# Optimization experiments

Hardware: AMD Instinct MI355X
Metric: run time of the kernel (lower is better)

The kernel has to match this reference:

```python
import jax, jax.numpy as jnp
import numpy as np

HEAD_SIZE = 64


def setup_inputs() -> dict:
    key = jax.random.key(0)
    ks = jax.random.split(key, 4)
    B, S, H, D = 8, 4096, 768, HEAD_SIZE
    scale = 1.0 / np.sqrt(H)
    return {
        "x": jax.random.normal(ks[0], (B, S, H), dtype=jnp.float32),
        "Wq": jax.random.normal(ks[1], (H, D), dtype=jnp.float32) * scale,
        "bq": jnp.zeros((D,), dtype=jnp.float32),
        "Wk": jax.random.normal(ks[2], (H, D), dtype=jnp.float32) * scale,
        "bk": jnp.zeros((D,), dtype=jnp.float32),
        "Wv": jax.random.normal(ks[3], (H, D), dtype=jnp.float32) * scale,
        "bv": jnp.zeros((D,), dtype=jnp.float32),
    }


def reference(x, Wq, bq, Wk, bk, Wv, bv):
    # x: [B, S, H]
    B, S, H = x.shape
    D = Wq.shape[1]
    q = x @ Wq + bq  # [B, S, D]
    k = x @ Wk + bk
    v = x @ Wv + bv
    # naive full score matrix [B, S, S]
    scores = jnp.einsum("bsd,btd->bst", q, k)
    causal = jnp.tril(jnp.ones((S, S), dtype=bool))  # lower-triangular mask
    scores = jnp.where(causal[None, :, :], scores, -jnp.inf)
    attn = jax.nn.softmax(scores / jnp.sqrt(jnp.float32(D)), axis=-1)
    # dropout is identity in eval/deterministic reference
    out = jnp.einsum("bst,btd->bsd", attn, v)  # [B, S, D]
    return out
```

## Files before the change

kernel.cpp:

```cpp
#include <hip/hip_runtime.h>

typedef unsigned short u16;
typedef __bf16 bf16_t;
typedef bf16_t bf16x8 __attribute__((ext_vector_type(8)));
typedef float f32x4 __attribute__((ext_vector_type(4)));
typedef u16 u16x8 __attribute__((ext_vector_type(8)));
typedef u16 u16x4 __attribute__((ext_vector_type(4)));

#define B_ 8
#define S_ 4096
#define H_ 768
#define M_ (B_ * S_)

__device__ __forceinline__ u16 f2b(float f) {
  unsigned u = __float_as_uint(f);
  u += 0x7fffu + ((u >> 16) & 1u);
  return (u16)(u >> 16);
}

__device__ __forceinline__ void gl_lds16(const void* g, void* l) {
  __builtin_amdgcn_global_load_lds(
      (const __attribute__((address_space(1))) void*)g,
      (__attribute__((address_space(3))) void*)l, 16, 0, 0);
}

__global__ __launch_bounds__(256) void wconv_k(const float* __restrict__ Wq,
                                               const float* __restrict__ Wk,
                                               const float* __restrict__ Wv,
                                               u16* __restrict__ WbT) {
  __shared__ float wt[64 * 68];
  const int tid = threadIdx.x;
  int mat = blockIdx.x / 12;
  int k0 = (blockIdx.x % 12) * 64;
  const float* W = (mat == 0) ? Wq : ((mat == 1) ? Wk : Wv);
  int r = tid >> 2, c0 = (tid & 3) * 16;
  const float* src = W + (size_t)(k0 + r) * 64 + c0;
#pragma unroll
  for (int j = 0; j < 16; j += 4)
    *(float4*)&wt[r * 68 + c0 + j] = *(const float4*)(src + j);
  __syncthreads();
  int d = tid >> 2;
  u16* dst = WbT + (size_t)(mat * 64 + d) * 768 + k0 + c0;
  u16x8 o0, o1;
#pragma unroll
  for (int j = 0; j < 8; ++j) o0[j] = f2b(wt[(c0 + j) * 68 + d]);
#pragma unroll
  for (int j = 0; j < 8; ++j) o1[j] = f2b(wt[(c0 + 8 + j) * 68 + d]);
  *(u16x8*)dst = o0;
  *(u16x8*)(dst + 8) = o1;
}

__global__ __launch_bounds__(256) void qkv_k(const float* __restrict__ x,
                                             const u16* __restrict__ WbT,
                                             const float* __restrict__ bq,
                                             const float* __restrict__ bk,
                                             const float* __restrict__ bv,
                                             u16* __restrict__ qb,
                                             u16* __restrict__ kb,
                                             u16* __restrict__ vbT) {
  __shared__ __align__(16) u16 smem[2 * 2560 + 2 * 7680];
  const int tid = threadIdx.x;
  const int w = tid >> 6, ln = tid & 15, qd = (tid >> 4) & 3;
  const int row0 = blockIdx.x * 64;

  const f32x4 z4 = {0.f, 0.f, 0.f, 0.f};
  f32x4 acc[4][3];
#pragma unroll
  for (int rt = 0; rt < 4; ++rt)
#pragma unroll
    for (int ct = 0; ct < 3; ++ct) acc[rt][ct] = z4;

  const int xr = tid >> 2, xc = (tid & 3) * 8;
  float4 xf0, xf1;
  u16x8 wf[3];

  auto load_t = [&](int kt) {
    const float* sx = x + (size_t)(row0 + xr) * 768 + kt * 32 + xc;
    xf0 = *(const float4*)sx;
    xf1 = *(const float4*)(sx + 4);
#pragma unroll
    for (int i = 0; i < 3; ++i) {
      int c = i * 256 + tid;
      int r = c >> 2, off = (c & 3) * 8;
      wf[i] = *(const u16x8*)(WbT + (size_t)r * 768 + kt * 32 + off);
    }
  };
  auto write_b = [&](int kt) {
    u16* xs = smem + (kt & 1) * 2560;
    u16* wsb = smem + 5120 + (kt & 1) * 7680;
    u16x8 v;
    v[0] = f2b(xf0.x); v[1] = f2b(xf0.y); v[2] = f2b(xf0.z); v[3] = f2b(xf0.w);
    v[4] = f2b(xf1.x); v[5] = f2b(xf1.y); v[6] = f2b(xf1.z); v[7] = f2b(xf1.w);
    *(u16x8*)&xs[xr * 40 + xc] = v;
#pragma unroll
    for (int i = 0; i < 3; ++i) {
      int c = i * 256 + tid;
      int r = c >> 2, off = (c & 3) * 8;
      *(u16x8*)&wsb[r * 40 + off] = wf[i];
    }
  };

  load_t(0);
  write_b(0);
  load_t(1);
  for (int kt = 0; kt < 24; ++kt) {
    __syncthreads();
    if (kt < 23) {
      write_b(kt + 1);
      if (kt < 22) load_t(kt + 2);
    }
    u16* xs = smem + (kt & 1) * 2560;
    u16* wsb = smem + 5120 + (kt & 1) * 7680;
    bf16x8 af[4], bfr[3];
#pragma unroll
    for (int rt = 0; rt < 4; ++rt)
      af[rt] = *(const bf16x8*)&xs[(rt * 16 + ln) * 40 + qd * 8];
#pragma unroll
    for (int ct = 0; ct < 3; ++ct)
      bfr[ct] = *(const bf16x8*)&wsb[(w * 48 + ct * 16 + ln) * 40 + qd * 8];
#pragma unroll
    for (int rt = 0; rt < 4; ++rt)
#pragma unroll
      for (int ct = 0; ct < 3; ++ct)
        acc[rt][ct] = __builtin_amdgcn_mfma_f32_16x16x32_bf16(
            af[rt], bfr[ct], acc[rt][ct], 0, 0, 0);
    __syncthreads();
  }

  u16* vt = smem;
#pragma unroll
  for (int ct = 0; ct < 3; ++ct) {
    int col = w * 48 + ct * 16 + ln;
    int mat = col >> 6, d = col & 63;
    if (mat < 2) {
      const float* bp = (mat == 0) ? bq : bk;
      u16* op = (mat == 0) ? qb : kb;
      float bias = bp[d];
      float scale = (mat == 0) ? 0.18033688011112042f : 1.0f;
#pragma unroll
      for (int rt = 0; rt < 4; ++rt)
#pragma unroll
        for (int r = 0; r < 4; ++r)
          op[(size_t)(row0 + rt * 16 + qd * 4 + r) * 64 + d] =
              f2b((acc[rt][ct][r] + bias) * scale);
    } else {
      float bias = bv[d];
#pragma unroll
      for (int rt = 0; rt < 4; ++rt)
#pragma unroll
        for (int r = 0; r < 4; ++r)
          vt[d * 72 + rt * 16 + qd * 4 + r] = f2b(acc[rt][ct][r] + bias);
    }
  }
  __syncthreads();
  {
    int d = tid >> 2, so = (tid & 3) * 16;
    int b = row0 >> 12, s0 = row0 & 4095;
    u16* dst = vbT + ((size_t)b * 64 + d) * 4096 + s0 + so;
    *(u16x8*)dst = *(const u16x8*)&vt[d * 72 + so];
    *(u16x8*)(dst + 8) = *(const u16x8*)&vt[d * 72 + so + 8];
  }
}

__global__ __launch_bounds__(256, 2) void attn_k(const u16* __restrict__ qb,
                                                 const u16* __restrict__ kb,
                                                 const u16* __restrict__ vbT,
                                                 u16* __restrict__ po,
                                                 float* __restrict__ pl) {
  __shared__ __align__(16) u16 ks[2][4096];
  __shared__ __align__(16) u16 vs[2][4096];
  __shared__ __align__(16) u16 ps[4 * 16 * 72];
  const int tid = threadIdx.x;
  const int w = tid >> 6, ln = tid & 15, qd = (tid >> 4) & 3;
  const int id = blockIdx.x;
  const int b = id & 7;
  int t = id >> 3;
  int qi = 15, rem = t;
  for (;;) {
    int c = (4 * qi + 11) >> 3;
    if (rem < c) break;
    rem -= c;
    --qi;
  }
  const int chunk = rem;
  const int tstart = rem * 8;
  int tcount = 4 * qi + 4 - tstart;
  if (tcount > 8) tcount = 8;
  const int q0 = qi * 256, q0w = q0 + w * 64;
  const int base = b * S_;
  const u16* kg = kb + (size_t)base * 64;
  const u16* vg = vbT + (size_t)b * 64 * 4096;

  bf16x8 qf[4][2];
#pragma unroll
  for (int qt = 0; qt < 4; ++qt) {
    const u16* qrow = qb + (size_t)(base + q0w + qt * 16 + ln) * 64;
    qf[qt][0] = *(const bf16x8*)(qrow + qd * 8);
    qf[qt][1] = *(const bf16x8*)(qrow + 32 + qd * 8);
  }
  const f32x4 z4 = {0.f, 0.f, 0.f, 0.f};
  f32x4 o[4][4];
#pragma unroll
  for (int qt = 0; qt < 4; ++qt)
#pragma unroll
    for (int nt = 0; nt < 4; ++nt) o[qt][nt] = z4;
  float lp[4] = {0.f, 0.f, 0.f, 0.f};
  u16* psw = ps + w * (16 * 72);
  const int lr = (tid & 63) >> 3, csl = tid & 7;

  auto prefetch = [&](int bufi, int tile) {
    const u16* kt_ = kg + (size_t)tile * 4096;
    const u16* vt_ = vg + tile * 64;
#pragma unroll
    for (int i = 0; i < 2; ++i) {
      int r0 = w * 16 + i * 8;
      int r = r0 + lr;
      int c = csl ^ (r & 7);
      gl_lds16(kt_ + r * 64 + c * 8, &ks[bufi][r0 * 64]);
      gl_lds16(vt_ + (size_t)r * 4096 + c * 8, &vs[bufi][r0 * 64]);
    }
  };

  prefetch(0, tstart);
  int buf = 0;
  for (int it = 0; it < tcount; ++it) {
    __syncthreads();
    if (it + 1 < tcount) prefetch(buf ^ 1, tstart + it + 1);
    const int t0a = (tstart + it) * 64;

    bf16x8 kf[2][4], vf[2][4];
#pragma unroll
    for (int kc = 0; kc < 2; ++kc) {
      int cs = ((kc * 4 + qd) ^ (ln & 7)) * 8;
#pragma unroll
      for (int nt = 0; nt < 4; ++nt) {
        kf[kc][nt] = *(const bf16x8*)&ks[buf][(nt * 16 + ln) * 64 + cs];
        vf[kc][nt] = *(const bf16x8*)&vs[buf][(nt * 16 + ln) * 64 + cs];
      }
    }
#pragma unroll
    for (int qt = 0; qt < 4; ++qt) {
      f32x4 s[4] = {z4, z4, z4, z4};
#pragma unroll
      for (int kc = 0; kc < 2; ++kc)
#pragma unroll
        for (int nt = 0; nt < 4; ++nt)
          s[nt] = __builtin_amdgcn_mfma_f32_16x16x32_bf16(kf[kc][nt], qf[qt][kc],
                                                          s[nt], 0, 0, 0);
      if (t0a + 63 > q0w + qt * 16) {
#pragma unroll
        for (int nt = 0; nt < 4; ++nt) {
          int tg = t0a + nt * 16 + qd * 4;
          int qg = q0w + qt * 16 + ln;
#pragma unroll
          for (int r = 0; r < 4; ++r)
            if (tg + r > qg) s[nt][r] = -INFINITY;
        }
      }
#pragma unroll
      for (int nt = 0; nt < 4; ++nt) {
        u16x4 pk;
#pragma unroll
        for (int r = 0; r < 4; ++r) {
          float p = __builtin_amdgcn_exp2f(s[nt][r]);
          lp[qt] += p;
          pk[r] = f2b(p);
        }
        *(u16x4*)&psw[ln * 72 + nt * 16 + qd * 4] = pk;
      }
#pragma unroll
      for (int kc = 0; kc < 2; ++kc) {
        bf16x8 pf = *(const bf16x8*)&psw[ln * 72 + kc * 32 + qd * 8];
#pragma unroll
        for (int nt = 0; nt < 4; ++nt)
          o[qt][nt] = __builtin_amdgcn_mfma_f32_16x16x32_bf16(vf[kc][nt], pf,
                                                              o[qt][nt], 0, 0, 0);
      }
    }
    buf ^= 1;
  }

  u16* poc = po + (size_t)chunk * M_ * 64;
  float* plc = pl + (size_t)chunk * M_;
#pragma unroll
  for (int qt = 0; qt < 4; ++qt) {
    float v = lp[qt];
    v += __shfl_xor(v, 16);
    v += __shfl_xor(v, 32);
    int row = base + q0w + qt * 16 + ln;
#pragma unroll
    for (int nt = 0; nt < 4; ++nt) {
      u16x4 ov;
#pragma unroll
      for (int r = 0; r < 4; ++r) ov[r] = f2b(o[qt][nt][r]);
      *(u16x4*)&poc[(size_t)row * 64 + nt * 16 + qd * 4] = ov;
    }
    if (qd == 0) plc[row] = v;
  }
}

__global__ __launch_bounds__(256) void comb_k(const u16* __restrict__ po,
                                              const float* __restrict__ pl,
                                              float* __restrict__ out) {
  int idx = blockIdx.x * 256 + threadIdx.x;
  int r = idx >> 4, d0 = (idx & 15) * 4;
  int qi = (r & 4095) >> 8;
  int nch = (4 * qi + 11) >> 3;
  float4 a = {0.f, 0.f, 0.f, 0.f};
  float l = 0.f;
  for (int c = 0; c < nch; ++c) {
    u16x4 p = *(const u16x4*)(po + ((size_t)c * M_ + r) * 64 + d0);
    a.x += __uint_as_float((unsigned)p[0] << 16);
    a.y += __uint_as_float((unsigned)p[1] << 16);
    a.z += __uint_as_float((unsigned)p[2] << 16);
    a.w += __uint_as_float((unsigned)p[3] << 16);
    l += pl[(size_t)c * M_ + r];
  }
  float inv = 1.0f / l;
  a.x *= inv; a.y *= inv; a.z *= inv; a.w *= inv;
  *(float4*)(out + (size_t)r * 64 + d0) = a;
}

extern "C" void kernel_launch(void* const* d_in, const int* in_sizes, int n_in,
                              void* d_out, int out_size, void* d_ws, size_t ws_size,
                              hipStream_t stream) {
  const float* x  = (const float*)d_in[0];
  const float* Wq = (const float*)d_in[1];
  const float* bq = (const float*)d_in[2];
  const float* Wk = (const float*)d_in[3];
  const float* bk = (const float*)d_in[4];
  const float* Wv = (const float*)d_in[5];
  const float* bv = (const float*)d_in[6];
  float* out = (float*)d_out;

  char* wsp = (char*)d_ws;
  u16* WbT  = (u16*)wsp;
  u16* qb   = (u16*)(wsp + 294912);
  u16* kb   = (u16*)(wsp + 4489216);
  u16* vbT  = (u16*)(wsp + 8683520);
  u16* po   = (u16*)(wsp + 12877824);
  float* pl = (float*)(wsp + 46432256);

  hipLaunchKernelGGL(wconv_k, dim3(36), dim3(256), 0, stream, Wq, Wk, Wv, WbT);
  hipLaunchKernelGGL(qkv_k, dim3(512), dim3(256), 0, stream,
                     x, WbT, bq, bk, bv, qb, kb, vbT);
  hipLaunchKernelGGL(attn_k, dim3(576), dim3(256), 0, stream,
                     qb, kb, vbT, po, pl);
  hipLaunchKernelGGL(comb_k, dim3(2048), dim3(256), 0, stream, po, pl, out);
}
```

Baseline: 230.8 us.

## Drop LDS staging in QKV and attention, load MFMA fragments directly from global

The QKV projection kernel drops its double-buffered LDS tiles. Each wave now loads x rows and all 192 weight columns straight into registers and accumulates a 16x192 strip, with a higher occupancy hint. V is stored in a per-64-token tiled transposed layout so the attention kernel can fetch K and V fragments directly from global memory into register double buffers (A/B ping-pong) instead of global_load_lds into swizzled LDS. This removes barriers and LDS traffic but relies on L1/L2 to serve the redundant per-wave global loads, and it raises register pressure.

```diff
diff --git a/kernel.cpp b/kernel.cpp
--- a/kernel.cpp
+++ b/kernel.cpp
@@ -16,12 +16,6 @@
   unsigned u = __float_as_uint(f);
   u += 0x7fffu + ((u >> 16) & 1u);
   return (u16)(u >> 16);
-}
-
-__device__ __forceinline__ void gl_lds16(const void* g, void* l) {
-  __builtin_amdgcn_global_load_lds(
-      (const __attribute__((address_space(1))) void*)g,
-      (__attribute__((address_space(3))) void*)l, 16, 0, 0);
 }
 
 __global__ __launch_bounds__(256) void wconv_k(const float* __restrict__ Wq,
@@ -50,125 +44,84 @@
   *(u16x8*)(dst + 8) = o1;
 }
 
-__global__ __launch_bounds__(256) void qkv_k(const float* __restrict__ x,
-                                             const u16* __restrict__ WbT,
-                                             const float* __restrict__ bq,
-                                             const float* __restrict__ bk,
-                                             const float* __restrict__ bv,
-                                             u16* __restrict__ qb,
-                                             u16* __restrict__ kb,
-                                             u16* __restrict__ vbT) {
-  __shared__ __align__(16) u16 smem[2 * 2560 + 2 * 7680];
+__global__ __launch_bounds__(256, 4) void qkv_k(const float* __restrict__ x,
+                                                const u16* __restrict__ WbT,
+                                                const float* __restrict__ bq,
+                                                const float* __restrict__ bk,
+                                                const float* __restrict__ bv,
+                                                u16* __restrict__ qb,
+                                                u16* __restrict__ kb,
+                                                u16* __restrict__ vbT2) {
+  __shared__ __align__(16) u16 vt[64 * 72];
   const int tid = threadIdx.x;
   const int w = tid >> 6, ln = tid & 15, qd = (tid >> 4) & 3;
-  const int row0 = blockIdx.x * 64;
+  const int r0 = blockIdx.x * 64 + w * 16;
 
   const f32x4 z4 = {0.f, 0.f, 0.f, 0.f};
-  f32x4 acc[4][3];
-#pragma unroll
-  for (int rt = 0; rt < 4; ++rt)
-#pragma unroll
-    for (int ct = 0; ct < 3; ++ct) acc[rt][ct] = z4;
-
-  const int xr = tid >> 2, xc = (tid & 3) * 8;
-  float4 xf0, xf1;
-  u16x8 wf[3];
-
-  auto load_t = [&](int kt) {
-    const float* sx = x + (size_t)(row0 + xr) * 768 + kt * 32 + xc;
-    xf0 = *(const float4*)sx;
-    xf1 = *(const float4*)(sx + 4);
-#pragma unroll
-    for (int i = 0; i < 3; ++i) {
-      int c = i * 256 + tid;
-      int r = c >> 2, off = (c & 3) * 8;
-      wf[i] = *(const u16x8*)(WbT + (size_t)r * 768 + kt * 32 + off);
-    }
-  };
-  auto write_b = [&](int kt) {
-    u16* xs = smem + (kt & 1) * 2560;
-    u16* wsb = smem + 5120 + (kt & 1) * 7680;
-    u16x8 v;
-    v[0] = f2b(xf0.x); v[1] = f2b(xf0.y); v[2] = f2b(xf0.z); v[3] = f2b(xf0.w);
-    v[4] = f2b(xf1.x); v[5] = f2b(xf1.y); v[6] = f2b(xf1.z); v[7] = f2b(xf1.w);
-    *(u16x8*)&xs[xr * 40 + xc] = v;
-#pragma unroll
-    for (int i = 0; i < 3; ++i) {
-      int c = i * 256 + tid;
-      int r = c >> 2, off = (c & 3) * 8;
-      *(u16x8*)&wsb[r * 40 + off] = wf[i];
-    }
-  };
-
-  load_t(0);
-  write_b(0);
-  load_t(1);
+  f32x4 acc[12];
+#pragma unroll
+  for (int ct = 0; ct < 12; ++ct) acc[ct] = z4;
+
+  const float* xrow = x + (size_t)(r0 + ln) * 768 + qd * 8;
+  const u16* wrow = WbT + (size_t)ln * 768 + qd * 8;
+
   for (int kt = 0; kt < 24; ++kt) {
-    __syncthreads();
-    if (kt < 23) {
-      write_b(kt + 1);
-      if (kt < 22) load_t(kt + 2);
-    }
-    u16* xs = smem + (kt & 1) * 2560;
-    u16* wsb = smem + 5120 + (kt & 1) * 7680;
-    bf16x8 af[4], bfr[3];
-#pragma unroll
-    for (int rt = 0; rt < 4; ++rt)
-      af[rt] = *(const bf16x8*)&xs[(rt * 16 + ln) * 40 + qd * 8];
-#pragma unroll
-    for (int ct = 0; ct < 3; ++ct)
-      bfr[ct] = *(const bf16x8*)&wsb[(w * 48 + ct * 16 + ln) * 40 + qd * 8];
-#pragma unroll
-    for (int rt = 0; rt < 4; ++rt)
-#pragma unroll
-      for (int ct = 0; ct < 3; ++ct)
-        acc[rt][ct] = __builtin_amdgcn_mfma_f32_16x16x32_bf16(
-            af[rt], bfr[ct], acc[rt][ct], 0, 0, 0);
-    __syncthreads();
-  }
-
-  u16* vt = smem;
-#pragma unroll
-  for (int ct = 0; ct < 3; ++ct) {
-    int col = w * 48 + ct * 16 + ln;
-    int mat = col >> 6, d = col & 63;
-    if (mat < 2) {
-      const float* bp = (mat == 0) ? bq : bk;
-      u16* op = (mat == 0) ? qb : kb;
-      float bias = bp[d];
-      float scale = (mat == 0) ? 0.18033688011112042f : 1.0f;
-#pragma unroll
-      for (int rt = 0; rt < 4; ++rt)
-#pragma unroll
-        for (int r = 0; r < 4; ++r)
-          op[(size_t)(row0 + rt * 16 + qd * 4 + r) * 64 + d] =
-              f2b((acc[rt][ct][r] + bias) * scale);
-    } else {
-      float bias = bv[d];
-#pragma unroll
-      for (int rt = 0; rt < 4; ++rt)
-#pragma unroll
-        for (int r = 0; r < 4; ++r)
-          vt[d * 72 + rt * 16 + qd * 4 + r] = f2b(acc[rt][ct][r] + bias);
-    }
+    float4 a0 = *(const float4*)(xrow + kt * 32);
+    float4 a1 = *(const float4*)(xrow + kt * 32 + 4);
+    u16x8 wv[12];
+#pragma unroll
+    for (int ct = 0; ct < 12; ++ct)
+      wv[ct] = *(const u16x8*)(wrow + (size_t)ct * 12288 + kt * 32);
+    u16x8 af;
+    af[0] = f2b(a0.x); af[1] = f2b(a0.y); af[2] = f2b(a0.z); af[3] = f2b(a0.w);
+    af[4] = f2b(a1.x); af[5] = f2b(a1.y); af[6] = f2b(a1.z); af[7] = f2b(a1.w);
+    bf16x8 afb = (bf16x8)af;
+#pragma unroll
+    for (int ct = 0; ct < 12; ++ct)
+      acc[ct] = __builtin_amdgcn_mfma_f32_16x16x32_bf16(afb, (bf16x8)wv[ct],
+                                                        acc[ct], 0, 0, 0);
+  }
+
+  const float scq = 0.18033688011112042f;
+#pragma unroll
+  for (int ct = 0; ct < 4; ++ct) {
+    float bias = bq[ct * 16 + ln];
+#pragma unroll
+    for (int r = 0; r < 4; ++r)
+      qb[(size_t)(r0 + qd * 4 + r) * 64 + ct * 16 + ln] =
+          f2b((acc[ct][r] + bias) * scq);
+  }
+#pragma unroll
+  for (int ct = 4; ct < 8; ++ct) {
+    float bias = bk[(ct - 4) * 16 + ln];
+#pragma unroll
+    for (int r = 0; r < 4; ++r)
+      kb[(size_t)(r0 + qd * 4 + r) * 64 + (ct - 4) * 16 + ln] =
+          f2b(acc[ct][r] + bias);
+  }
+#pragma unroll
+  for (int ct = 8; ct < 12; ++ct) {
+    float bias = bv[(ct - 8) * 16 + ln];
+    int d = (ct - 8) * 16 + ln;
+#pragma unroll
+    for (int r = 0; r < 4; ++r)
+      vt[d * 72 + w * 16 + qd * 4 + r] = f2b(acc[ct][r] + bias);
   }
   __syncthreads();
   {
-    int d = tid >> 2, so = (tid & 3) * 16;
-    int b = row0 >> 12, s0 = row0 & 4095;
-    u16* dst = vbT + ((size_t)b * 64 + d) * 4096 + s0 + so;
-    *(u16x8*)dst = *(const u16x8*)&vt[d * 72 + so];
-    *(u16x8*)(dst + 8) = *(const u16x8*)&vt[d * 72 + so + 8];
+    int d = tid >> 2, t0l = (tid & 3) * 16;
+    int b = blockIdx.x >> 6, ti = blockIdx.x & 63;
+    u16* dst = vbT2 + (size_t)(b * 64 + ti) * 4096 + d * 64 + t0l;
+    *(u16x8*)dst = *(const u16x8*)&vt[d * 72 + t0l];
+    *(u16x8*)(dst + 8) = *(const u16x8*)&vt[d * 72 + t0l + 8];
   }
 }
 
 __global__ __launch_bounds__(256, 2) void attn_k(const u16* __restrict__ qb,
                                                  const u16* __restrict__ kb,
-                                                 const u16* __restrict__ vbT,
+                                                 const u16* __restrict__ vbT2,
                                                  u16* __restrict__ po,
                                                  float* __restrict__ pl) {
-  __shared__ __align__(16) u16 ks[2][4096];
-  __shared__ __align__(16) u16 vs[2][4096];
   __shared__ __align__(16) u16 ps[4 * 16 * 72];
   const int tid = threadIdx.x;
   const int w = tid >> 6, ln = tid & 15, qd = (tid >> 4) & 3;
@@ -189,7 +142,7 @@
   const int q0 = qi * 256, q0w = q0 + w * 64;
   const int base = b * S_;
   const u16* kg = kb + (size_t)base * 64;
-  const u16* vg = vbT + (size_t)b * 64 * 4096;
+  const u16* vg = vbT2 + (size_t)b * 64 * 4096;
 
   bf16x8 qf[4][2];
 #pragma unroll
@@ -206,38 +159,22 @@
     for (int nt = 0; nt < 4; ++nt) o[qt][nt] = z4;
   float lp[4] = {0.f, 0.f, 0.f, 0.f};
   u16* psw = ps + w * (16 * 72);
-  const int lr = (tid & 63) >> 3, csl = tid & 7;
-
-  auto prefetch = [&](int bufi, int tile) {
+
+  bf16x8 kA[2][4], vA[2][4], kB[2][4], vB[2][4];
+
+  auto ldtile = [&](bf16x8(&kf)[2][4], bf16x8(&vf)[2][4], int tile) {
     const u16* kt_ = kg + (size_t)tile * 4096;
-    const u16* vt_ = vg + tile * 64;
-#pragma unroll
-    for (int i = 0; i < 2; ++i) {
-      int r0 = w * 16 + i * 8;
-      int r = r0 + lr;
-      int c = csl ^ (r & 7);
-      gl_lds16(kt_ + r * 64 + c * 8, &ks[bufi][r0 * 64]);
-      gl_lds16(vt_ + (size_t)r * 4096 + c * 8, &vs[bufi][r0 * 64]);
-    }
+    const u16* vt_ = vg + (size_t)tile * 4096;
+#pragma unroll
+    for (int kc = 0; kc < 2; ++kc)
+#pragma unroll
+      for (int nt = 0; nt < 4; ++nt) {
+        kf[kc][nt] = *(const bf16x8*)(kt_ + (nt * 16 + ln) * 64 + kc * 32 + qd * 8);
+        vf[kc][nt] = *(const bf16x8*)(vt_ + (nt * 16 + ln) * 64 + kc * 32 + qd * 8);
+      }
   };
 
-  prefetch(0, tstart);
-  int buf = 0;
-  for (int it = 0; it < tcount; ++it) {
-    __syncthreads();
-    if (it + 1 < tcount) prefetch(buf ^ 1, tstart + it + 1);
-    const int t0a = (tstart + it) * 64;
-
-    bf16x8 kf[2][4], vf[2][4];
-#pragma unroll
-    for (int kc = 0; kc < 2; ++kc) {
-      int cs = ((kc * 4 + qd) ^ (ln & 7)) * 8;
-#pragma unroll
-      for (int nt = 0; nt < 4; ++nt) {
-        kf[kc][nt] = *(const bf16x8*)&ks[buf][(nt * 16 + ln) * 64 + cs];
-        vf[kc][nt] = *(const bf16x8*)&vs[buf][(nt * 16 + ln) * 64 + cs];
-      }
-    }
+  auto body = [&](const bf16x8(&kf)[2][4], const bf16x8(&vf)[2][4], int t0a) {
 #pragma unroll
     for (int qt = 0; qt < 4; ++qt) {
       f32x4 s[4] = {z4, z4, z4, z4};
@@ -277,7 +214,19 @@
                                                               o[qt][nt], 0, 0, 0);
       }
     }
-    buf ^= 1;
+  };
+
+  ldtile(kA, vA, tstart);
+  int it = 0;
+  for (;;) {
+    if (it + 1 < tcount) ldtile(kB, vB, tstart + it + 1);
+    body(kA, vA, (tstart + it) * 64);
+    ++it;
+    if (it >= tcount) break;
+    if (it + 1 < tcount) ldtile(kA, vA, tstart + it + 1);
+    body(kB, vB, (tstart + it) * 64);
+    ++it;
+    if (it >= tcount) break;
   }
 
   u16* poc = po + (size_t)chunk * M_ * 64;
@@ -337,14 +286,14 @@
   u16* WbT  = (u16*)wsp;
   u16* qb   = (u16*)(wsp + 294912);
   u16* kb   = (u16*)(wsp + 4489216);
-  u16* vbT  = (u16*)(wsp + 8683520);
+  u16* vbT2 = (u16*)(wsp + 8683520);
   u16* po   = (u16*)(wsp + 12877824);
   float* pl = (float*)(wsp + 46432256);
 
   hipLaunchKernelGGL(wconv_k, dim3(36), dim3(256), 0, stream, Wq, Wk, Wv, WbT);
   hipLaunchKernelGGL(qkv_k, dim3(512), dim3(256), 0, stream,
-                     x, WbT, bq, bk, bv, qb, kb, vbT);
+                     x, WbT, bq, bk, bv, qb, kb, vbT2);
   hipLaunchKernelGGL(attn_k, dim3(576), dim3(256), 0, stream,
-                     qb, kb, vbT, po, pl);
+                     qb, kb, vbT2, po, pl);
   hipLaunchKernelGGL(comb_k, dim3(2048), dim3(256), 0, stream, po, pl, out);
 }
```

After: 422.6 us. 83.1% more time.
